# Kernel optimization log

Measured on AMD Instinct MI355X. Metric: run time of the kernel, lower is better.

Reference implementation:

```python
import jax, jax.numpy as jnp
import numpy as np

N = 50000      # nodes
E = 800000     # edges (avg degree 16)
DIN = 128
HID = 128
OUT = 10       # classes
G = 64         # graphs in batch


def setup_inputs() -> dict:
    key = jax.random.key(0)
    ks = jax.random.split(key, 10)
    x = jax.random.normal(ks[0], (N, DIN), dtype=jnp.float32)
    edge_index = jax.random.randint(ks[1], (2, E), 0, N, dtype=jnp.int32)
    edge_weight = jax.random.uniform(ks[2], (E,), dtype=jnp.float32)
    batch = jnp.sort(jax.random.randint(ks[3], (N,), 0, G, dtype=jnp.int32))
    W1 = jax.random.normal(ks[4], (DIN, HID), dtype=jnp.float32) / np.sqrt(DIN)
    b1 = jnp.zeros((HID,), dtype=jnp.float32)
    W2 = jax.random.normal(ks[5], (HID, HID), dtype=jnp.float32) / np.sqrt(HID)
    b2 = jnp.zeros((HID,), dtype=jnp.float32)
    W3 = jax.random.normal(ks[6], (HID, OUT), dtype=jnp.float32) / np.sqrt(HID)
    b3 = jnp.zeros((OUT,), dtype=jnp.float32)
    return {"x": x, "edge_index": edge_index, "edge_weight": edge_weight,
            "batch": batch, "W1": W1, "b1": b1, "W2": W2, "b2": b2,
            "W3": W3, "b3": b3}


def _gcn_norm(edge_index, edge_weight, n_nodes):
    # PyG gcn_norm: add self-loops with weight 1, D^-1/2 (A+I) D^-1/2
    loop = jnp.arange(n_nodes, dtype=edge_index.dtype)
    src = jnp.concatenate([edge_index[0], loop])
    dst = jnp.concatenate([edge_index[1], loop])
    w = jnp.concatenate([edge_weight, jnp.ones((n_nodes,), edge_weight.dtype)])
    deg = jax.ops.segment_sum(w, dst, num_segments=n_nodes)
    dinv = jnp.where(deg > 0, jax.lax.rsqrt(deg), 0.0)
    norm = dinv[src] * w * dinv[dst]
    return src, dst, norm


def _gcn_conv(x, W, b, src, dst, norm, n_nodes):
    h = x @ W                                      # [N, F] dense transform
    msg = norm[:, None] * h[src]                   # gather + scale  [E+N, F]
    out = jax.ops.segment_sum(msg, dst, num_segments=n_nodes)  # scatter-add
    return out + b


def reference(x, edge_index, edge_weight, batch, W1, b1, W2, b2, W3, b3):
    src, dst, norm = _gcn_norm(edge_index, edge_weight, N)
    h = jax.nn.relu(_gcn_conv(x, W1, b1, src, dst, norm, N))
    h = jax.nn.relu(_gcn_conv(h, W2, b2, src, dst, norm, N))
    h = _gcn_conv(h, W3, b3, src, dst, norm, N)    # [N, OUT]
    # global_mean_pool over graph ids
    sums = jax.ops.segment_sum(h, batch, num_segments=G)          # [G, OUT]
    cnts = jax.ops.segment_sum(jnp.ones((N,), h.dtype), batch, num_segments=G)
    pooled = sums / jnp.maximum(cnts, 1.0)[:, None]
    return jax.nn.log_softmax(pooled, axis=1)
```

## Files before the change

### kernel.cpp

```cpp
#include <hip/hip_runtime.h>
#include <math.h>

#define NN 50000
#define EE 800000
#define GG 64
#define FD 128
#define OUTD 10
#define GB 782
#define BB 196
#define NBU 196
#define NBK 128
#define CH 6250
#define RCAP 8

typedef __attribute__((ext_vector_type(8))) short s8v;
typedef __attribute__((ext_vector_type(4))) float f4v;

static __device__ inline unsigned short f2b(float f) {
    unsigned int u = __float_as_uint(f);
    return (unsigned short)((u + 0x7FFFu + ((u >> 16) & 1u)) >> 16);
}


__global__ void k_prep(const float* __restrict__ W1, const float* __restrict__ W2,
                       const float* __restrict__ W3, unsigned short* __restrict__ Wt1,
                       unsigned short* __restrict__ Wt2, float* __restrict__ W3t) {
    int i = blockIdx.x * blockDim.x + threadIdx.x;
    if (i < FD * FD) {
        int nn = i >> 7, k = i & 127;
        Wt1[i] = f2b(W1[k * FD + nn]);
        Wt2[i] = f2b(W2[k * FD + nn]);
    }
    if (i < FD * OUTD) {
        int col = i >> 7, row = i & 127;
        W3t[i] = W3[row * OUTD + col];
    }
}


static __device__ inline void gemm_f32in_body(int bid, const float* __restrict__ A,
        const unsigned short* __restrict__ Wt, unsigned short* __restrict__ out, int n) {
    int tid = threadIdx.x;
    int wave = tid >> 6, lane = tid & 63;
    int quad = lane >> 4, c16 = lane & 15;
    int rowbase = bid * 64 + wave * 16;
    int rowA = rowbase + c16;
    if (rowA >= n) rowA = n - 1;
    f4v acc[8];
    #pragma unroll
    for (int t = 0; t < 8; ++t) acc[t] = (f4v){0.f, 0.f, 0.f, 0.f};
    #pragma unroll
    for (int k0 = 0; k0 < 128; k0 += 32) {
        const float* ap = A + (size_t)rowA * FD + k0 + quad * 8;
        float4 a0 = *(const float4*)ap;
        float4 a1 = *(const float4*)(ap + 4);
        s8v a;
        a[0] = (short)f2b(a0.x); a[1] = (short)f2b(a0.y);
        a[2] = (short)f2b(a0.z); a[3] = (short)f2b(a0.w);
        a[4] = (short)f2b(a1.x); a[5] = (short)f2b(a1.y);
        a[6] = (short)f2b(a1.z); a[7] = (short)f2b(a1.w);
        #pragma unroll
        for (int t = 0; t < 8; ++t) {
            s8v b = *(const s8v*)(Wt + (size_t)(t * 16 + c16) * FD + k0 + quad * 8);
            acc[t] = __builtin_amdgcn_mfma_f32_16x16x32_bf16(a, b, acc[t], 0, 0, 0);
        }
    }
    #pragma unroll
    for (int t = 0; t < 8; ++t) {
        #pragma unroll
        for (int r = 0; r < 4; ++r) {
            int row = rowbase + quad * 4 + r;
            if (row < n) out[(size_t)row * FD + t * 16 + c16] = f2b(acc[t][r]);
        }
    }
}

__global__ __launch_bounds__(256) void k_megaA(const float* __restrict__ x,
        const unsigned short* __restrict__ Wt1, unsigned short* __restrict__ hA,
        const int* __restrict__ dst, int* __restrict__ cnt2d,
        const int* __restrict__ batch, int* __restrict__ gstart) {
    int b = blockIdx.x;
    int tid = threadIdx.x;
    if (b < GB) {
        gemm_f32in_body(b, x, Wt1, hA, NN);
    } else if (b < GB + NBK) {
        __shared__ unsigned hist[NBU];
        int blk = b - GB;
        if (tid < NBU) hist[tid] = 0;
        __syncthreads();
        int e0 = blk * CH;
        for (int e = e0 + tid; e < e0 + CH; e += 256)
            atomicAdd(&hist[(unsigned)dst[e] >> 8], 1u);
        __syncthreads();
        if (tid < NBU) cnt2d[tid * NBK + blk] = (int)hist[tid];
    } else {
        int i = (b - GB - NBK) * 256 + tid;
        if (i < NN) {
            int bb = batch[i];
            int bp = (i == 0) ? -1 : batch[i - 1];
            for (int g = bp + 1; g <= bb; ++g) gstart[g] = i;
            if (i == NN - 1)
                for (int g = bb + 1; g <= GG; ++g) gstart[g] = NN;
        }
    }
}


__global__ __launch_bounds__(256) void k_scatter(const int* __restrict__ src,
        const int* __restrict__ dst, const float* __restrict__ ew,
        const int* __restrict__ cnt2d, int* __restrict__ bbase_g,
        uint2* __restrict__ rec) {
    __shared__ int colsum[NBU];
    __shared__ int ownoff[NBU];
    __shared__ unsigned cur[NBU];
    __shared__ int wtot_s[4];
    int tid = threadIdx.x;
    int blk = blockIdx.x;
    if (tid < NBU) {
        const int* c = cnt2d + tid * NBK;
        int own = 0, tot = 0;
        for (int b = 0; b < NBK; ++b) {
            int t = c[b];
            if (b < blk) own += t;
            tot += t;
        }
        ownoff[tid] = own;
        colsum[tid] = tot;
    }
    __syncthreads();
    {
        int lane = tid & 63, wv = tid >> 6;
        int v = (tid < NBU) ? colsum[tid] : 0;
        int s = v;
        #pragma unroll
        for (int off = 1; off < 64; off <<= 1) {
            int u = __shfl_up(s, off, 64);
            if (lane >= off) s += u;
        }
        if (lane == 63) wtot_s[wv] = s;
        __syncthreads();
        int pre = 0;
        for (int j = 0; j < wv; ++j) pre += wtot_s[j];
        int base = pre + s - v;
        if (tid < NBU) {
            cur[tid] = (unsigned)(base + ownoff[tid]);
            if (blk == 0) bbase_g[tid] = base;
        }
        if (blk == 0 && tid == NBU - 1) bbase_g[NBU] = base + v;
    }
    __syncthreads();
    int e0 = blk * CH;
    for (int e = e0 + tid; e < e0 + CH; e += 256) {
        int d = dst[e];
        unsigned bkt = (unsigned)d >> 8;
        unsigned pos = atomicAdd(&cur[bkt], 1u);
        rec[pos] = make_uint2(((unsigned)(d & 255) << 16) | (unsigned)src[e],
                              __float_as_uint(ew[e]));
    }
}


__global__ __launch_bounds__(1024) void k_rankfill(const uint2* __restrict__ rec,
        const int* __restrict__ bbase, int* __restrict__ rowptr, float* __restrict__ dinv_g,
        uint2* __restrict__ ent, unsigned short* __restrict__ rankb) {
    __shared__ unsigned cntS[256];
    __shared__ float wdegS[256];
    __shared__ int wtot_s[4];
    __shared__ int rowS[256];
    __shared__ float dinvS[256];
    int b = blockIdx.x;
    int tid = threadIdx.x;
    if (tid < 256) { cntS[tid] = 0; wdegS[tid] = 0.0f; }
    __syncthreads();
    int beg = bbase[b], end = bbase[b + 1];
    int s0 = beg + tid;
    uint2 rv[RCAP];
    unsigned rk[RCAP];
    #pragma unroll
    for (int k = 0; k < RCAP; ++k) {
        int s = s0 + k * 1024;
        if (s < end) {
            uint2 r = rec[s];
            unsigned dl = r.x >> 16;
            unsigned old = atomicAdd(&cntS[dl], 1u);
            atomicAdd(&wdegS[dl], __uint_as_float(r.y));
            rv[k] = r; rk[k] = old;
        }
    }
    for (int s = s0 + RCAP * 1024; s < end; s += 1024) {
        uint2 r = rec[s];
        unsigned dl = r.x >> 16;
        unsigned old = atomicAdd(&cntS[dl], 1u);
        atomicAdd(&wdegS[dl], __uint_as_float(r.y));
        rankb[s] = (unsigned short)old;
    }
    __syncthreads();
    {
        int lane = tid & 63, wv = tid >> 6;
        int v = (tid < 256) ? (int)cntS[tid] : 0;
        int s = v;
        #pragma unroll
        for (int off = 1; off < 64; off <<= 1) {
            int u = __shfl_up(s, off, 64);
            if (lane >= off) s += u;
        }
        if (tid < 256 && lane == 63) wtot_s[wv] = s;
        __syncthreads();
        if (tid < 256) {
            int pre = 0;
            for (int j = 0; j < wv; ++j) pre += wtot_s[j];
            int excl = pre + s - v;
            int node = b * 256 + tid;
            if (node < NN) {
                int r = beg + node + excl;
                rowS[tid] = r;
                rowptr[node] = r;
                float di = 1.0f / sqrtf(wdegS[tid] + 1.0f);
                dinvS[tid] = di;
                dinv_g[node] = di;
                ent[r + v] = make_uint2((unsigned)node, __float_as_uint(di));
            }
            if (node == NN - 1) rowptr[NN] = EE + NN;
        }
    }
    __syncthreads();
    #pragma unroll
    for (int k = 0; k < RCAP; ++k) {
        int s = s0 + k * 1024;
        if (s < end) {
            uint2 r = rv[k];
            unsigned dl = r.x >> 16;
            int pos = rowS[dl] + (int)rk[k];
            float val = __uint_as_float(r.y) * dinvS[dl];
            ent[pos] = make_uint2(r.x & 0xFFFFu, __float_as_uint(val));
        }
    }
    for (int s = s0 + RCAP * 1024; s < end; s += 1024) {
        uint2 r = rec[s];
        unsigned dl = r.x >> 16;
        int pos = rowS[dl] + (int)rankb[s];
        float val = __uint_as_float(r.y) * dinvS[dl];
        ent[pos] = make_uint2(r.x & 0xFFFFu, __float_as_uint(val));
    }
}


__global__ __launch_bounds__(256) void k_gemm_bf(const unsigned short* __restrict__ A,
        const unsigned short* __restrict__ Wt, unsigned short* __restrict__ out, int n) {
    int tid = threadIdx.x;
    int wave = tid >> 6, lane = tid & 63;
    int quad = lane >> 4, c16 = lane & 15;
    int rowbase = blockIdx.x * 64 + wave * 16;
    int rowA = rowbase + c16;
    if (rowA >= n) rowA = n - 1;
    f4v acc[8];
    #pragma unroll
    for (int t = 0; t < 8; ++t) acc[t] = (f4v){0.f, 0.f, 0.f, 0.f};
    #pragma unroll
    for (int k0 = 0; k0 < 128; k0 += 32) {
        s8v a = *(const s8v*)(A + (size_t)rowA * FD + k0 + quad * 8);
        #pragma unroll
        for (int t = 0; t < 8; ++t) {
            s8v b = *(const s8v*)(Wt + (size_t)(t * 16 + c16) * FD + k0 + quad * 8);
            acc[t] = __builtin_amdgcn_mfma_f32_16x16x32_bf16(a, b, acc[t], 0, 0, 0);
        }
    }
    #pragma unroll
    for (int t = 0; t < 8; ++t) {
        #pragma unroll
        for (int r = 0; r < 4; ++r) {
            int row = rowbase + quad * 4 + r;
            if (row < n) out[(size_t)row * FD + t * 16 + c16] = f2b(acc[t][r]);
        }
    }
}


__global__ __launch_bounds__(256) void k_spmm_bf(const int* __restrict__ rowptr,
        const uint2* __restrict__ ent, const float* __restrict__ dinv,
        const unsigned short* __restrict__ tin, const float* __restrict__ bias,
        unsigned short* __restrict__ out, int n, int dorelu) {
    int w = (blockIdx.x * blockDim.x + threadIdx.x) >> 6;
    int lane = threadIdx.x & 63;
    if (w >= n) return;
    int c = lane & 15, g = lane >> 4;
    int beg = rowptr[w], end = rowptr[w + 1];
    float acc[8];
    #pragma unroll
    for (int j = 0; j < 8; ++j) acc[j] = 0.0f;
    int e0 = beg;
    for (; e0 + 16 <= end; e0 += 16) {
        uint2 en[4];
        float dv[4];
        uint4 t[4];
        #pragma unroll
        for (int u = 0; u < 4; ++u) en[u] = ent[e0 + 4 * u + g];
        #pragma unroll
        for (int u = 0; u < 4; ++u) dv[u] = dinv[en[u].x];
        #pragma unroll
        for (int u = 0; u < 4; ++u)
            t[u] = *(const uint4*)(tin + (size_t)en[u].x * FD + c * 8);
        #pragma unroll
        for (int u = 0; u < 4; ++u) {
            float v = __uint_as_float(en[u].y) * dv[u];
            acc[0] += v * __uint_as_float(t[u].x << 16);
            acc[1] += v * __uint_as_float(t[u].x & 0xFFFF0000u);
            acc[2] += v * __uint_as_float(t[u].y << 16);
            acc[3] += v * __uint_as_float(t[u].y & 0xFFFF0000u);
            acc[4] += v * __uint_as_float(t[u].z << 16);
            acc[5] += v * __uint_as_float(t[u].z & 0xFFFF0000u);
            acc[6] += v * __uint_as_float(t[u].w << 16);
            acc[7] += v * __uint_as_float(t[u].w & 0xFFFF0000u);
        }
    }
    for (; e0 < end; e0 += 4) {
        int e = e0 + g;
        uint2 en = (e < end) ? ent[e] : make_uint2(0u, 0u);
        float v = (e < end) ? __uint_as_float(en.y) * dinv[en.x] : 0.0f;
        uint4 t = *(const uint4*)(tin + (size_t)en.x * FD + c * 8);
        acc[0] += v * __uint_as_float(t.x << 16);
        acc[1] += v * __uint_as_float(t.x & 0xFFFF0000u);
        acc[2] += v * __uint_as_float(t.y << 16);
        acc[3] += v * __uint_as_float(t.y & 0xFFFF0000u);
        acc[4] += v * __uint_as_float(t.z << 16);
        acc[5] += v * __uint_as_float(t.z & 0xFFFF0000u);
        acc[6] += v * __uint_as_float(t.w << 16);
        acc[7] += v * __uint_as_float(t.w & 0xFFFF0000u);
    }
    #pragma unroll
    for (int j = 0; j < 8; ++j) {
        acc[j] += __shfl_xor(acc[j], 16, 64);
        acc[j] += __shfl_xor(acc[j], 32, 64);
    }
    if (g == 0) {
        uint4 r;
        float o[8];
        #pragma unroll
        for (int j = 0; j < 8; ++j) {
            float x = acc[j] + bias[c * 8 + j];
            o[j] = dorelu ? fmaxf(x, 0.0f) : x;
        }
        r.x = (unsigned)f2b(o[0]) | ((unsigned)f2b(o[1]) << 16);
        r.y = (unsigned)f2b(o[2]) | ((unsigned)f2b(o[3]) << 16);
        r.z = (unsigned)f2b(o[4]) | ((unsigned)f2b(o[5]) << 16);
        r.w = (unsigned)f2b(o[6]) | ((unsigned)f2b(o[7]) << 16);
        *(uint4*)(out + (size_t)w * FD + c * 8) = r;
    }
}

__global__ __launch_bounds__(256) void k_spmm_w3(const int* __restrict__ rowptr,
        const uint2* __restrict__ ent, const float* __restrict__ dinv,
        const unsigned short* __restrict__ tin, const float* __restrict__ bias2,
        const float* __restrict__ W3t, float* __restrict__ outc, int n) {
    int tid = threadIdx.x;
    int w = (blockIdx.x * blockDim.x + tid) >> 6;
    int lane = tid & 63;
    if (w >= n) return;
    int c = lane & 15, g = lane >> 4;
    int beg = rowptr[w], end = rowptr[w + 1];
    float acc[8];
    #pragma unroll
    for (int j = 0; j < 8; ++j) acc[j] = 0.0f;
    int e0 = beg;
    for (; e0 + 16 <= end; e0 += 16) {
        uint2 en[4];
        float dv[4];
        uint4 t[4];
        #pragma unroll
        for (int u = 0; u < 4; ++u) en[u] = ent[e0 + 4 * u + g];
        #pragma unroll
        for (int u = 0; u < 4; ++u) dv[u] = dinv[en[u].x];
        #pragma unroll
        for (int u = 0; u < 4; ++u)
            t[u] = *(const uint4*)(tin + (size_t)en[u].x * FD + c * 8);
        #pragma unroll
        for (int u = 0; u < 4; ++u) {
            float v = __uint_as_float(en[u].y) * dv[u];
            acc[0] += v * __uint_as_float(t[u].x << 16);
            acc[1] += v * __uint_as_float(t[u].x & 0xFFFF0000u);
            acc[2] += v * __uint_as_float(t[u].y << 16);
            acc[3] += v * __uint_as_float(t[u].y & 0xFFFF0000u);
            acc[4] += v * __uint_as_float(t[u].z << 16);
            acc[5] += v * __uint_as_float(t[u].z & 0xFFFF0000u);
            acc[6] += v * __uint_as_float(t[u].w << 16);
            acc[7] += v * __uint_as_float(t[u].w & 0xFFFF0000u);
        }
    }
    for (; e0 < end; e0 += 4) {
        int e = e0 + g;
        uint2 en = (e < end) ? ent[e] : make_uint2(0u, 0u);
        float v = (e < end) ? __uint_as_float(en.y) * dinv[en.x] : 0.0f;
        uint4 t = *(const uint4*)(tin + (size_t)en.x * FD + c * 8);
        acc[0] += v * __uint_as_float(t.x << 16);
        acc[1] += v * __uint_as_float(t.x & 0xFFFF0000u);
        acc[2] += v * __uint_as_float(t.y << 16);
        acc[3] += v * __uint_as_float(t.y & 0xFFFF0000u);
        acc[4] += v * __uint_as_float(t.z << 16);
        acc[5] += v * __uint_as_float(t.z & 0xFFFF0000u);
        acc[6] += v * __uint_as_float(t.w << 16);
        acc[7] += v * __uint_as_float(t.w & 0xFFFF0000u);
    }
    #pragma unroll
    for (int j = 0; j < 8; ++j) {
        acc[j] += __shfl_xor(acc[j], 16, 64);
        acc[j] += __shfl_xor(acc[j], 32, 64);
    }
    float b2r[8], o[8];
    *(float4*)&b2r[0] = *(const float4*)(bias2 + c * 8);
    *(float4*)&b2r[4] = *(const float4*)(bias2 + c * 8 + 4);
    #pragma unroll
    for (int j = 0; j < 8; ++j)
        o[j] = fmaxf(acc[j] + b2r[j], 0.0f);
    float w0[8], w1[8];
    *(float4*)&w0[0] = *(const float4*)(W3t + g * FD + c * 8);
    *(float4*)&w0[4] = *(const float4*)(W3t + g * FD + c * 8 + 4);
    *(float4*)&w1[0] = *(const float4*)(W3t + (g + 4) * FD + c * 8);
    *(float4*)&w1[4] = *(const float4*)(W3t + (g + 4) * FD + c * 8 + 4);
    float p0 = 0.0f, p1 = 0.0f, p2 = 0.0f;
    #pragma unroll
    for (int j = 0; j < 8; ++j) {
        p0 += o[j] * w0[j];
        p1 += o[j] * w1[j];
    }
    if (g < 2) {
        float w2[8];
        *(float4*)&w2[0] = *(const float4*)(W3t + (g + 8) * FD + c * 8);
        *(float4*)&w2[4] = *(const float4*)(W3t + (g + 8) * FD + c * 8 + 4);
        #pragma unroll
        for (int j = 0; j < 8; ++j) p2 += o[j] * w2[j];
    }
    #pragma unroll
    for (int off = 1; off < 16; off <<= 1) {
        p0 += __shfl_xor(p0, off, 64);
        p1 += __shfl_xor(p1, off, 64);
        p2 += __shfl_xor(p2, off, 64);
    }
    if (c == 0) {
        float* op = outc + (size_t)w * OUTD;
        op[g] = p0;
        op[g + 4] = p1;
        if (g < 2) op[g + 8] = p2;
    }
}

__global__ void k_spmm10(const int* __restrict__ rowptr, const uint2* __restrict__ ent,
        const float* __restrict__ dinv, const float* __restrict__ tin,
        const float* __restrict__ bias, float* __restrict__ out, int n) {
    int t = blockIdx.x * blockDim.x + threadIdx.x;
    int node = t / OUTD;
    int c = t - node * OUTD;
    if (node >= n) return;
    int beg = rowptr[node], end = rowptr[node + 1];
    float acc = 0.0f;
    for (int e = beg; e < end; ++e) {
        uint2 en = ent[e];
        acc += __uint_as_float(en.y) * dinv[en.x] * tin[(size_t)en.x * OUTD + c];
    }
    out[(size_t)node * OUTD + c] = acc + bias[c];
}


__global__ __launch_bounds__(256) void k_poolfin(const float* __restrict__ h,
        const int* __restrict__ gstart, float* __restrict__ out) {
    int g = blockIdx.x;
    int beg = gstart[g], end = gstart[g + 1];
    int tid = threadIdx.x;
    int lane = tid & 63, wv = tid >> 6;
    float acc[OUTD];
    #pragma unroll
    for (int c = 0; c < OUTD; ++c) acc[c] = 0.0f;
    for (int i = beg + tid; i < end; i += 256) {
        const float* hp = h + (size_t)i * OUTD;
        #pragma unroll
        for (int c = 0; c < OUTD; ++c) acc[c] += hp[c];
    }
    #pragma unroll
    for (int off = 32; off >= 1; off >>= 1)
        #pragma unroll
        for (int c = 0; c < OUTD; ++c) acc[c] += __shfl_down(acc[c], off, 64);
    __shared__ float ws[4][OUTD];
    if (lane == 0)
        #pragma unroll
        for (int c = 0; c < OUTD; ++c) ws[wv][c] = acc[c];
    __syncthreads();
    if (tid == 0) {
        float cf = fmaxf((float)(end - beg), 1.0f);
        float v[OUTD], m = -1e30f;
        #pragma unroll
        for (int c = 0; c < OUTD; ++c) {
            v[c] = (ws[0][c] + ws[1][c] + ws[2][c] + ws[3][c]) / cf;
            m = fmaxf(m, v[c]);
        }
        float s = 0.0f;
        #pragma unroll
        for (int c = 0; c < OUTD; ++c) s += expf(v[c] - m);
        float l = logf(s);
        #pragma unroll
        for (int c = 0; c < OUTD; ++c) out[g * OUTD + c] = v[c] - m - l;
    }
}


extern "C" void kernel_launch(void* const* d_in, const int* in_sizes, int n_in,
                              void* d_out, int out_size, void* d_ws, size_t ws_size,
                              hipStream_t stream) {
    const float* x   = (const float*)d_in[0];
    const int*   ei  = (const int*)d_in[1];
    const float* ew  = (const float*)d_in[2];
    const int*   bat = (const int*)d_in[3];
    const float* W1  = (const float*)d_in[4];
    const float* b1  = (const float*)d_in[5];
    const float* W2  = (const float*)d_in[6];
    const float* b2  = (const float*)d_in[7];
    const float* W3  = (const float*)d_in[8];
    const float* b3  = (const float*)d_in[9];
    float* out = (float*)d_out;

    const int* src = ei;
    const int* dst = ei + EE;

    char* p = (char*)d_ws;
    auto alloc = [&](size_t bytes) -> void* {
        void* r = (void*)p;
        p += (bytes + 255) & ~(size_t)255;
        return r;
    };
    int*            cnt2d  = (int*)  alloc((size_t)NBU * NBK * 4);
    int*            bbase  = (int*)  alloc((size_t)(NBU + 1) * 4);
    uint2*          rec    = (uint2*)alloc((size_t)EE * 8);
    unsigned short* rankb  = (unsigned short*)alloc((size_t)EE * 2);
    float*          dinv   = (float*)alloc((size_t)NN * 4);
    int*            rowptr = (int*)  alloc((size_t)(NN + 1) * 4);
    uint2*          ent    = (uint2*)alloc((size_t)(EE + NN) * 8);
    unsigned short* Wt1    = (unsigned short*)alloc((size_t)FD * FD * 2);
    unsigned short* Wt2    = (unsigned short*)alloc((size_t)FD * FD * 2);
    float*          W3t    = (float*)alloc((size_t)FD * OUTD * 4);
    unsigned short* hA     = (unsigned short*)alloc((size_t)NN * FD * 2);
    unsigned short* hB     = (unsigned short*)alloc((size_t)NN * FD * 2);
    float*          bufC   = (float*)alloc((size_t)NN * OUTD * 4);
    float*          bufD   = (float*)alloc((size_t)NN * OUTD * 4);
    int*            gstart = (int*)  alloc((size_t)(GG + 1) * 4);
    (void)ws_size; (void)in_sizes; (void)n_in; (void)out_size;

    const int B = 256;
    k_prep    <<<(FD * FD + B - 1) / B, B, 0, stream>>>(W1, W2, W3, Wt1, Wt2, W3t);
    k_megaA   <<<GB + NBK + BB, B, 0, stream>>>(x, Wt1, hA, dst, cnt2d, bat, gstart);
    k_scatter <<<NBK, B, 0, stream>>>(src, dst, ew, cnt2d, bbase, rec);
    k_rankfill<<<NBU, 1024, 0, stream>>>(rec, bbase, rowptr, dinv, ent, rankb);

    k_spmm_bf <<<(NN * 64 + B - 1) / B, B, 0, stream>>>(rowptr, ent, dinv, hA, b1, hB, NN, 1);
    k_gemm_bf <<<GB, B, 0, stream>>>(hB, Wt2, hA, NN);
    k_spmm_w3 <<<(NN * 64 + B - 1) / B, B, 0, stream>>>(rowptr, ent, dinv, hA, b2, W3t, bufC, NN);
    k_spmm10  <<<(NN * OUTD + B - 1) / B, B, 0, stream>>>(rowptr, ent, dinv, bufC, b3, bufD, NN);
    k_poolfin <<<GG, 256, 0, stream>>>(bufD, gstart, out);
}
```

Before: 267.9 us.

## Fuse pooling into final SpMM and fold source dinv into producer epilogues

Merges weight prep with the histogram/graph-bounds kernel and the edge scatter with the first GEMM, cutting kernel launches. The final 10-wide aggregation now accumulates per-graph sums in shared memory and global atomics, and the last block computes mean pooling and log-softmax, removing the separate pool kernel and intermediate buffer. The dinv scaling of source nodes moves into the epilogues of the producing kernels, so the per-edge dinv gathers disappear. Risks: float atomic summation order becomes nondeterministic, and correctness depends on every producer applying the dinv scaling consistently.

After: 372.3 us. 38.9% more time.

```diff
diff --git a/kernel.cpp b/kernel.cpp
--- a/kernel.cpp
+++ b/kernel.cpp
@@ -12,6 +12,8 @@
 #define NBK 128
 #define CH 6250
 #define RCAP 8
+#define TB 64
+#define NPB 1954
 
 typedef __attribute__((ext_vector_type(8))) short s8v;
 typedef __attribute__((ext_vector_type(4))) float f4v;
@@ -22,18 +24,46 @@
 }
 
 
-__global__ void k_prep(const float* __restrict__ W1, const float* __restrict__ W2,
-                       const float* __restrict__ W3, unsigned short* __restrict__ Wt1,
-                       unsigned short* __restrict__ Wt2, float* __restrict__ W3t) {
-    int i = blockIdx.x * blockDim.x + threadIdx.x;
-    if (i < FD * FD) {
-        int nn = i >> 7, k = i & 127;
-        Wt1[i] = f2b(W1[k * FD + nn]);
-        Wt2[i] = f2b(W2[k * FD + nn]);
-    }
-    if (i < FD * OUTD) {
-        int col = i >> 7, row = i & 127;
-        W3t[i] = W3[row * OUTD + col];
+__global__ __launch_bounds__(256) void k_histbounds(const float* __restrict__ W1,
+        const float* __restrict__ W2, const float* __restrict__ W3,
+        unsigned short* __restrict__ Wt1, unsigned short* __restrict__ Wt2,
+        float* __restrict__ W3t, const int* __restrict__ dst, int* __restrict__ cnt2d,
+        const int* __restrict__ batch, int* __restrict__ gstart,
+        float* __restrict__ sums, int* __restrict__ done) {
+    int b = blockIdx.x;
+    int tid = threadIdx.x;
+    if (b < TB) {
+        int i = b * 256 + tid;
+        if (i < FD * FD) {
+            int nn = i >> 7, k = i & 127;
+            Wt1[i] = f2b(W1[k * FD + nn]);
+            Wt2[i] = f2b(W2[k * FD + nn]);
+        }
+        if (i < FD * OUTD) {
+            int col = i >> 7, row = i & 127;
+            W3t[i] = W3[row * OUTD + col];
+        }
+        if (i < GG * OUTD) sums[i] = 0.0f;
+        if (i == 1024) *done = 0;
+    } else if (b < TB + NBK) {
+        __shared__ unsigned hist[NBU];
+        int blk = b - TB;
+        if (tid < NBU) hist[tid] = 0;
+        __syncthreads();
+        int e0 = blk * CH;
+        for (int e = e0 + tid; e < e0 + CH; e += 256)
+            atomicAdd(&hist[(unsigned)dst[e] >> 8], 1u);
+        __syncthreads();
+        if (tid < NBU) cnt2d[tid * NBK + blk] = (int)hist[tid];
+    } else {
+        int i = (b - TB - NBK) * 256 + tid;
+        if (i < NN) {
+            int bb = batch[i];
+            int bp = (i == 0) ? -1 : batch[i - 1];
+            for (int g = bp + 1; g <= bb; ++g) gstart[g] = i;
+            if (i == NN - 1)
+                for (int g = bb + 1; g <= GG; ++g) gstart[g] = NN;
+        }
     }
 }
 
@@ -61,8 +91,8 @@
         a[6] = (short)f2b(a1.z); a[7] = (short)f2b(a1.w);
         #pragma unroll
         for (int t = 0; t < 8; ++t) {
-            s8v b = *(const s8v*)(Wt + (size_t)(t * 16 + c16) * FD + k0 + quad * 8);
-            acc[t] = __builtin_amdgcn_mfma_f32_16x16x32_bf16(a, b, acc[t], 0, 0, 0);
+            s8v bb = *(const s8v*)(Wt + (size_t)(t * 16 + c16) * FD + k0 + quad * 8);
+            acc[t] = __builtin_amdgcn_mfma_f32_16x16x32_bf16(a, bb, acc[t], 0, 0, 0);
         }
     }
     #pragma unroll
@@ -75,53 +105,28 @@
     }
 }
 
-__global__ __launch_bounds__(256) void k_megaA(const float* __restrict__ x,
-        const unsigned short* __restrict__ Wt1, unsigned short* __restrict__ hA,
-        const int* __restrict__ dst, int* __restrict__ cnt2d,
-        const int* __restrict__ batch, int* __restrict__ gstart) {
+__global__ __launch_bounds__(256) void k_scatgemm(const int* __restrict__ src,
+        const int* __restrict__ dst, const float* __restrict__ ew,
+        const int* __restrict__ cnt2d, int* __restrict__ bbase_g, uint2* __restrict__ rec,
+        const float* __restrict__ x, const unsigned short* __restrict__ Wt1,
+        unsigned short* __restrict__ hA) {
     int b = blockIdx.x;
     int tid = threadIdx.x;
-    if (b < GB) {
-        gemm_f32in_body(b, x, Wt1, hA, NN);
-    } else if (b < GB + NBK) {
-        __shared__ unsigned hist[NBU];
-        int blk = b - GB;
-        if (tid < NBU) hist[tid] = 0;
-        __syncthreads();
-        int e0 = blk * CH;
-        for (int e = e0 + tid; e < e0 + CH; e += 256)
-            atomicAdd(&hist[(unsigned)dst[e] >> 8], 1u);
-        __syncthreads();
-        if (tid < NBU) cnt2d[tid * NBK + blk] = (int)hist[tid];
-    } else {
-        int i = (b - GB - NBK) * 256 + tid;
-        if (i < NN) {
-            int bb = batch[i];
-            int bp = (i == 0) ? -1 : batch[i - 1];
-            for (int g = bp + 1; g <= bb; ++g) gstart[g] = i;
-            if (i == NN - 1)
-                for (int g = bb + 1; g <= GG; ++g) gstart[g] = NN;
-        }
-    }
-}
-
-
-__global__ __launch_bounds__(256) void k_scatter(const int* __restrict__ src,
-        const int* __restrict__ dst, const float* __restrict__ ew,
-        const int* __restrict__ cnt2d, int* __restrict__ bbase_g,
-        uint2* __restrict__ rec) {
+    if (b >= NBK) {
+        gemm_f32in_body(b - NBK, x, Wt1, hA, NN);
+        return;
+    }
     __shared__ int colsum[NBU];
     __shared__ int ownoff[NBU];
     __shared__ unsigned cur[NBU];
     __shared__ int wtot_s[4];
-    int tid = threadIdx.x;
-    int blk = blockIdx.x;
+    int blk = b;
     if (tid < NBU) {
         const int* c = cnt2d + tid * NBK;
         int own = 0, tot = 0;
-        for (int b = 0; b < NBK; ++b) {
-            int t = c[b];
-            if (b < blk) own += t;
+        for (int k = 0; k < NBK; ++k) {
+            int t = c[k];
+            if (k < blk) own += t;
             tot += t;
         }
         ownoff[tid] = own;
@@ -245,41 +250,10 @@
 }
 
 
-__global__ __launch_bounds__(256) void k_gemm_bf(const unsigned short* __restrict__ A,
-        const unsigned short* __restrict__ Wt, unsigned short* __restrict__ out, int n) {
-    int tid = threadIdx.x;
-    int wave = tid >> 6, lane = tid & 63;
-    int quad = lane >> 4, c16 = lane & 15;
-    int rowbase = blockIdx.x * 64 + wave * 16;
-    int rowA = rowbase + c16;
-    if (rowA >= n) rowA = n - 1;
-    f4v acc[8];
-    #pragma unroll
-    for (int t = 0; t < 8; ++t) acc[t] = (f4v){0.f, 0.f, 0.f, 0.f};
-    #pragma unroll
-    for (int k0 = 0; k0 < 128; k0 += 32) {
-        s8v a = *(const s8v*)(A + (size_t)rowA * FD + k0 + quad * 8);
-        #pragma unroll
-        for (int t = 0; t < 8; ++t) {
-            s8v b = *(const s8v*)(Wt + (size_t)(t * 16 + c16) * FD + k0 + quad * 8);
-            acc[t] = __builtin_amdgcn_mfma_f32_16x16x32_bf16(a, b, acc[t], 0, 0, 0);
-        }
-    }
-    #pragma unroll
-    for (int t = 0; t < 8; ++t) {
-        #pragma unroll
-        for (int r = 0; r < 4; ++r) {
-            int row = rowbase + quad * 4 + r;
-            if (row < n) out[(size_t)row * FD + t * 16 + c16] = f2b(acc[t][r]);
-        }
-    }
-}
-
-
 __global__ __launch_bounds__(256) void k_spmm_bf(const int* __restrict__ rowptr,
         const uint2* __restrict__ ent, const float* __restrict__ dinv,
         const unsigned short* __restrict__ tin, const float* __restrict__ bias,
-        unsigned short* __restrict__ out, int n, int dorelu) {
+        unsigned short* __restrict__ out, int n) {
     int w = (blockIdx.x * blockDim.x + threadIdx.x) >> 6;
     int lane = threadIdx.x & 63;
     if (w >= n) return;
@@ -333,13 +307,12 @@
         acc[j] += __shfl_xor(acc[j], 32, 64);
     }
     if (g == 0) {
+        float dself = dinv[w];
         uint4 r;
         float o[8];
         #pragma unroll
-        for (int j = 0; j < 8; ++j) {
-            float x = acc[j] + bias[c * 8 + j];
-            o[j] = dorelu ? fmaxf(x, 0.0f) : x;
-        }
+        for (int j = 0; j < 8; ++j)
+            o[j] = fmaxf(acc[j] + bias[c * 8 + j], 0.0f) * dself;
         r.x = (unsigned)f2b(o[0]) | ((unsigned)f2b(o[1]) << 16);
         r.y = (unsigned)f2b(o[2]) | ((unsigned)f2b(o[3]) << 16);
         r.z = (unsigned)f2b(o[4]) | ((unsigned)f2b(o[5]) << 16);
@@ -347,6 +320,38 @@
         *(uint4*)(out + (size_t)w * FD + c * 8) = r;
     }
 }
+
+
+__global__ __launch_bounds__(256) void k_gemm_bf(const unsigned short* __restrict__ A,
+        const unsigned short* __restrict__ Wt, unsigned short* __restrict__ out, int n) {
+    int tid = threadIdx.x;
+    int wave = tid >> 6, lane = tid & 63;
+    int quad = lane >> 4, c16 = lane & 15;
+    int rowbase = blockIdx.x * 64 + wave * 16;
+    int rowA = rowbase + c16;
+    if (rowA >= n) rowA = n - 1;
+    f4v acc[8];
+    #pragma unroll
+    for (int t = 0; t < 8; ++t) acc[t] = (f4v){0.f, 0.f, 0.f, 0.f};
+    #pragma unroll
+    for (int k0 = 0; k0 < 128; k0 += 32) {
+        s8v a = *(const s8v*)(A + (size_t)rowA * FD + k0 + quad * 8);
+        #pragma unroll
+        for (int t = 0; t < 8; ++t) {
+            s8v b = *(const s8v*)(Wt + (size_t)(t * 16 + c16) * FD + k0 + quad * 8);
+            acc[t] = __builtin_amdgcn_mfma_f32_16x16x32_bf16(a, b, acc[t], 0, 0, 0);
+        }
+    }
+    #pragma unroll
+    for (int t = 0; t < 8; ++t) {
+        #pragma unroll
+        for (int r = 0; r < 4; ++r) {
+            int row = rowbase + quad * 4 + r;
+            if (row < n) out[(size_t)row * FD + t * 16 + c16] = f2b(acc[t][r]);
+        }
+    }
+}
+
 
 __global__ __launch_bounds__(256) void k_spmm_w3(const int* __restrict__ rowptr,
         const uint2* __restrict__ ent, const float* __restrict__ dinv,
@@ -364,18 +369,15 @@
     int e0 = beg;
     for (; e0 + 16 <= end; e0 += 16) {
         uint2 en[4];
-        float dv[4];
         uint4 t[4];
         #pragma unroll
         for (int u = 0; u < 4; ++u) en[u] = ent[e0 + 4 * u + g];
-        #pragma unroll
-        for (int u = 0; u < 4; ++u) dv[u] = dinv[en[u].x];
         #pragma unroll
         for (int u = 0; u < 4; ++u)
             t[u] = *(const uint4*)(tin + (size_t)en[u].x * FD + c * 8);
         #pragma unroll
         for (int u = 0; u < 4; ++u) {
-            float v = __uint_as_float(en[u].y) * dv[u];
+            float v = __uint_as_float(en[u].y);
             acc[0] += v * __uint_as_float(t[u].x << 16);
             acc[1] += v * __uint_as_float(t[u].x & 0xFFFF0000u);
             acc[2] += v * __uint_as_float(t[u].y << 16);
@@ -389,7 +391,7 @@
     for (; e0 < end; e0 += 4) {
         int e = e0 + g;
         uint2 en = (e < end) ? ent[e] : make_uint2(0u, 0u);
-        float v = (e < end) ? __uint_as_float(en.y) * dinv[en.x] : 0.0f;
+        float v = (e < end) ? __uint_as_float(en.y) : 0.0f;
         uint4 t = *(const uint4*)(tin + (size_t)en.x * FD + c * 8);
         acc[0] += v * __uint_as_float(t.x << 16);
         acc[1] += v * __uint_as_float(t.x & 0xFFFF0000u);
@@ -436,67 +438,75 @@
         p2 += __shfl_xor(p2, off, 64);
     }
     if (c == 0) {
+        float dself = dinv[w];
         float* op = outc + (size_t)w * OUTD;
-        op[g] = p0;
-        op[g + 4] = p1;
-        if (g < 2) op[g + 8] = p2;
-    }
-}
-
-__global__ void k_spmm10(const int* __restrict__ rowptr, const uint2* __restrict__ ent,
-        const float* __restrict__ dinv, const float* __restrict__ tin,
-        const float* __restrict__ bias, float* __restrict__ out, int n) {
-    int t = blockIdx.x * blockDim.x + threadIdx.x;
+        op[g] = p0 * dself;
+        op[g + 4] = p1 * dself;
+        if (g < 2) op[g + 8] = p2 * dself;
+    }
+}
+
+
+__global__ __launch_bounds__(256) void k_spmm10pool(const int* __restrict__ rowptr,
+        const uint2* __restrict__ ent, const float* __restrict__ tin,
+        const float* __restrict__ bias, const int* __restrict__ batch,
+        const int* __restrict__ gstart, float* __restrict__ sums, int* __restrict__ done,
+        float* __restrict__ out) {
+    __shared__ float gs[16][OUTD];
+    __shared__ int gmin_s, gmax_s, last_s;
+    int tid = threadIdx.x;
+    int t = blockIdx.x * 256 + tid;
     int node = t / OUTD;
     int c = t - node * OUTD;
-    if (node >= n) return;
-    int beg = rowptr[node], end = rowptr[node + 1];
-    float acc = 0.0f;
-    for (int e = beg; e < end; ++e) {
-        uint2 en = ent[e];
-        acc += __uint_as_float(en.y) * dinv[en.x] * tin[(size_t)en.x * OUTD + c];
-    }
-    out[(size_t)node * OUTD + c] = acc + bias[c];
-}
-
-
-__global__ __launch_bounds__(256) void k_poolfin(const float* __restrict__ h,
-        const int* __restrict__ gstart, float* __restrict__ out) {
-    int g = blockIdx.x;
-    int beg = gstart[g], end = gstart[g + 1];
-    int tid = threadIdx.x;
-    int lane = tid & 63, wv = tid >> 6;
-    float acc[OUTD];
-    #pragma unroll
-    for (int c = 0; c < OUTD; ++c) acc[c] = 0.0f;
-    for (int i = beg + tid; i < end; i += 256) {
-        const float* hp = h + (size_t)i * OUTD;
-        #pragma unroll
-        for (int c = 0; c < OUTD; ++c) acc[c] += hp[c];
-    }
-    #pragma unroll
-    for (int off = 32; off >= 1; off >>= 1)
-        #pragma unroll
-        for (int c = 0; c < OUTD; ++c) acc[c] += __shfl_down(acc[c], off, 64);
-    __shared__ float ws[4][OUTD];
-    if (lane == 0)
-        #pragma unroll
-        for (int c = 0; c < OUTD; ++c) ws[wv][c] = acc[c];
-    __syncthreads();
-    if (tid == 0) {
-        float cf = fmaxf((float)(end - beg), 1.0f);
+    bool act = node < NN;
+    if (tid == 0) { gmin_s = 0x7fffffff; gmax_s = -1; }
+    if (tid < 16 * OUTD) gs[tid / OUTD][tid % OUTD] = 0.0f;
+    __syncthreads();
+    int g = 0;
+    float val = 0.0f;
+    if (act) {
+        g = batch[node];
+        atomicMin(&gmin_s, g);
+        atomicMax(&gmax_s, g);
+        int beg = rowptr[node], end = rowptr[node + 1];
+        for (int e = beg; e < end; ++e) {
+            uint2 en = ent[e];
+            val += __uint_as_float(en.y) * tin[(size_t)en.x * OUTD + c];
+        }
+        val += bias[c];
+    }
+    __syncthreads();
+    if (act) atomicAdd(&gs[g & 15][c], val);
+    __syncthreads();
+    if (tid < 16 * OUTD) {
+        int s = tid / OUTD, cc = tid - s * OUTD;
+        int gmin = gmin_s, gmax = gmax_s;
+        if (gmax >= 0) {
+            int gg = gmin + ((s - (gmin & 15) + 16) & 15);
+            if (gg <= gmax) atomicAdd(&sums[gg * OUTD + cc], gs[s][cc]);
+        }
+    }
+    __threadfence();
+    __syncthreads();
+    if (tid == 0) last_s = (atomicAdd(done, 1) == NPB - 1) ? 1 : 0;
+    __syncthreads();
+    if (last_s && tid < GG) {
+        int g2 = tid;
+        float cf = fmaxf((float)(gstart[g2 + 1] - gstart[g2]), 1.0f);
         float v[OUTD], m = -1e30f;
         #pragma unroll
-        for (int c = 0; c < OUTD; ++c) {
-            v[c] = (ws[0][c] + ws[1][c] + ws[2][c] + ws[3][c]) / cf;
-            m = fmaxf(m, v[c]);
+        for (int cc = 0; cc < OUTD; ++cc) {
+            float s = __hip_atomic_load(&sums[g2 * OUTD + cc], __ATOMIC_RELAXED,
+                                        __HIP_MEMORY_SCOPE_AGENT);
+            v[cc] = s / cf;
+            m = fmaxf(m, v[cc]);
         }
         float s = 0.0f;
         #pragma unroll
-        for (int c = 0; c < OUTD; ++c) s += expf(v[c] - m);
+        for (int cc = 0; cc < OUTD; ++cc) s += expf(v[cc] - m);
         float l = logf(s);
         #pragma unroll
-        for (int c = 0; c < OUTD; ++c) out[g * OUTD + c] = v[c] - m - l;
+        for (int cc = 0; cc < OUTD; ++cc) out[g2 * OUTD + cc] = v[cc] - m - l;
     }
 }
 
@@ -538,19 +548,18 @@
     unsigned short* hA     = (unsigned short*)alloc((size_t)NN * FD * 2);
     unsigned short* hB     = (unsigned short*)alloc((size_t)NN * FD * 2);
     float*          bufC   = (float*)alloc((size_t)NN * OUTD * 4);
-    float*          bufD   = (float*)alloc((size_t)NN * OUTD * 4);
+    float*          sums   = (float*)alloc((size_t)GG * OUTD * 4);
+    int*            done   = (int*)  alloc(256);
     int*            gstart = (int*)  alloc((size_t)(GG + 1) * 4);
     (void)ws_size; (void)in_sizes; (void)n_in; (void)out_size;
 
     const int B = 256;
-    k_prep    <<<(FD * FD + B - 1) / B, B, 0, stream>>>(W1, W2, W3, Wt1, Wt2, W3t);
-    k_megaA   <<<GB + NBK + BB, B, 0, stream>>>(x, Wt1, hA, dst, cnt2d, bat, gstart);
-    k_scatter <<<NBK, B, 0, stream>>>(src, dst, ew, cnt2d, bbase, rec);
-    k_rankfill<<<NBU, 1024, 0, stream>>>(rec, bbase, rowptr, dinv, ent, rankb);
-
-    k_spmm_bf <<<(NN * 64 + B - 1) / B, B, 0, stream>>>(rowptr, ent, dinv, hA, b1, hB, NN, 1);
-    k_gemm_bf <<<GB, B, 0, stream>>>(hB, Wt2, hA, NN);
-    k_spmm_w3 <<<(NN * 64 + B - 1) / B, B, 0, stream>>>(rowptr, ent, dinv, hA, b2, W3t, bufC, NN);
-    k_spmm10  <<<(NN * OUTD + B - 1) / B, B, 0, stream>>>(rowptr, ent, dinv, bufC, b3, bufD, NN);
-    k_poolfin <<<GG, 256, 0, stream>>>(bufD, gstart, out);
-}
+    k_histbounds<<<TB + NBK + BB, B, 0, stream>>>(W1, W2, W3, Wt1, Wt2, W3t,
+                                                  dst, cnt2d, bat, gstart, sums, done);
+    k_scatgemm  <<<NBK + GB, B, 0, stream>>>(src, dst, ew, cnt2d, bbase, rec, x, Wt1, hA);
+    k_rankfill  <<<NBU, 1024, 0, stream>>>(rec, bbase, rowptr, dinv, ent, rankb);
+    k_spmm_bf   <<<(NN * 64 + B - 1) / B, B, 0, stream>>>(rowptr, ent, dinv, hA, b1, hB, NN);
+    k_gemm_bf   <<<GB, B, 0, stream>>>(hB, Wt2, hA, NN);
+    k_spmm_w3   <<<(NN * 64 + B - 1) / B, B, 0, stream>>>(rowptr, ent, dinv, hA, b2, W3t, bufC, NN);
+    k_spmm10pool<<<NPB, B, 0, stream>>>(rowptr, ent, bufC, b3, bat, gstart, sums, done, out);
+}
```

## Fold source-side degree scaling into producers and merge setup kernels

Applied to the files above, without the earlier changes.

The source-side D^-1/2 factor is now applied once per row: the layer-1 and layer-2 aggregation epilogues multiply their outputs by dinv[node]. This lets the layer-2 and layer-3 aggregations drop the per-edge dinv gather, which is valid because the following GEMM is linear in row scaling. Weight preparation is merged into the histogram/graph-bounds kernel, and the first GEMM runs in the same launch as the edge scatter. That cuts the launch count and overlaps the dense GEMM with the irregular scatter. The extra dinv multiply before bf16 rounding slightly changes numerics.

After: 254.8 us. -4.9%, faster.

```diff
diff --git a/kernel.cpp b/kernel.cpp
--- a/kernel.cpp
+++ b/kernel.cpp
@@ -12,6 +12,7 @@
 #define NBK 128
 #define CH 6250
 #define RCAP 8
+#define TB 64
 
 typedef __attribute__((ext_vector_type(8))) short s8v;
 typedef __attribute__((ext_vector_type(4))) float f4v;
@@ -22,18 +23,43 @@
 }
 
 
-__global__ void k_prep(const float* __restrict__ W1, const float* __restrict__ W2,
-                       const float* __restrict__ W3, unsigned short* __restrict__ Wt1,
-                       unsigned short* __restrict__ Wt2, float* __restrict__ W3t) {
-    int i = blockIdx.x * blockDim.x + threadIdx.x;
-    if (i < FD * FD) {
-        int nn = i >> 7, k = i & 127;
-        Wt1[i] = f2b(W1[k * FD + nn]);
-        Wt2[i] = f2b(W2[k * FD + nn]);
-    }
-    if (i < FD * OUTD) {
-        int col = i >> 7, row = i & 127;
-        W3t[i] = W3[row * OUTD + col];
+__global__ __launch_bounds__(256) void k_histbounds(const float* __restrict__ W1,
+        const float* __restrict__ W2, const float* __restrict__ W3,
+        unsigned short* __restrict__ Wt1, unsigned short* __restrict__ Wt2,
+        float* __restrict__ W3t, const int* __restrict__ dst, int* __restrict__ cnt2d,
+        const int* __restrict__ batch, int* __restrict__ gstart) {
+    int b = blockIdx.x;
+    int tid = threadIdx.x;
+    if (b < TB) {
+        int i = b * 256 + tid;
+        if (i < FD * FD) {
+            int nn = i >> 7, k = i & 127;
+            Wt1[i] = f2b(W1[k * FD + nn]);
+            Wt2[i] = f2b(W2[k * FD + nn]);
+        }
+        if (i < FD * OUTD) {
+            int col = i >> 7, row = i & 127;
+            W3t[i] = W3[row * OUTD + col];
+        }
+    } else if (b < TB + NBK) {
+        __shared__ unsigned hist[NBU];
+        int blk = b - TB;
+        if (tid < NBU) hist[tid] = 0;
+        __syncthreads();
+        int e0 = blk * CH;
+        for (int e = e0 + tid; e < e0 + CH; e += 256)
+            atomicAdd(&hist[(unsigned)dst[e] >> 8], 1u);
+        __syncthreads();
+        if (tid < NBU) cnt2d[tid * NBK + blk] = (int)hist[tid];
+    } else {
+        int i = (b - TB - NBK) * 256 + tid;
+        if (i < NN) {
+            int bb = batch[i];
+            int bp = (i == 0) ? -1 : batch[i - 1];
+            for (int g = bp + 1; g <= bb; ++g) gstart[g] = i;
+            if (i == NN - 1)
+                for (int g = bb + 1; g <= GG; ++g) gstart[g] = NN;
+        }
     }
 }
 
@@ -61,8 +87,8 @@
         a[6] = (short)f2b(a1.z); a[7] = (short)f2b(a1.w);
         #pragma unroll
         for (int t = 0; t < 8; ++t) {
-            s8v b = *(const s8v*)(Wt + (size_t)(t * 16 + c16) * FD + k0 + quad * 8);
-            acc[t] = __builtin_amdgcn_mfma_f32_16x16x32_bf16(a, b, acc[t], 0, 0, 0);
+            s8v bb = *(const s8v*)(Wt + (size_t)(t * 16 + c16) * FD + k0 + quad * 8);
+            acc[t] = __builtin_amdgcn_mfma_f32_16x16x32_bf16(a, bb, acc[t], 0, 0, 0);
         }
     }
     #pragma unroll
@@ -75,53 +101,28 @@
     }
 }
 
-__global__ __launch_bounds__(256) void k_megaA(const float* __restrict__ x,
-        const unsigned short* __restrict__ Wt1, unsigned short* __restrict__ hA,
-        const int* __restrict__ dst, int* __restrict__ cnt2d,
-        const int* __restrict__ batch, int* __restrict__ gstart) {
+__global__ __launch_bounds__(256) void k_scatgemm(const int* __restrict__ src,
+        const int* __restrict__ dst, const float* __restrict__ ew,
+        const int* __restrict__ cnt2d, int* __restrict__ bbase_g, uint2* __restrict__ rec,
+        const float* __restrict__ x, const unsigned short* __restrict__ Wt1,
+        unsigned short* __restrict__ hA) {
     int b = blockIdx.x;
     int tid = threadIdx.x;
-    if (b < GB) {
-        gemm_f32in_body(b, x, Wt1, hA, NN);
-    } else if (b < GB + NBK) {
-        __shared__ unsigned hist[NBU];
-        int blk = b - GB;
-        if (tid < NBU) hist[tid] = 0;
-        __syncthreads();
-        int e0 = blk * CH;
-        for (int e = e0 + tid; e < e0 + CH; e += 256)
-            atomicAdd(&hist[(unsigned)dst[e] >> 8], 1u);
-        __syncthreads();
-        if (tid < NBU) cnt2d[tid * NBK + blk] = (int)hist[tid];
-    } else {
-        int i = (b - GB - NBK) * 256 + tid;
-        if (i < NN) {
-            int bb = batch[i];
-            int bp = (i == 0) ? -1 : batch[i - 1];
-            for (int g = bp + 1; g <= bb; ++g) gstart[g] = i;
-            if (i == NN - 1)
-                for (int g = bb + 1; g <= GG; ++g) gstart[g] = NN;
-        }
-    }
-}
-
-
-__global__ __launch_bounds__(256) void k_scatter(const int* __restrict__ src,
-        const int* __restrict__ dst, const float* __restrict__ ew,
-        const int* __restrict__ cnt2d, int* __restrict__ bbase_g,
-        uint2* __restrict__ rec) {
+    if (b >= NBK) {
+        gemm_f32in_body(b - NBK, x, Wt1, hA, NN);
+        return;
+    }
     __shared__ int colsum[NBU];
     __shared__ int ownoff[NBU];
     __shared__ unsigned cur[NBU];
     __shared__ int wtot_s[4];
-    int tid = threadIdx.x;
-    int blk = blockIdx.x;
+    int blk = b;
     if (tid < NBU) {
         const int* c = cnt2d + tid * NBK;
         int own = 0, tot = 0;
-        for (int b = 0; b < NBK; ++b) {
-            int t = c[b];
-            if (b < blk) own += t;
+        for (int k = 0; k < NBK; ++k) {
+            int t = c[k];
+            if (k < blk) own += t;
             tot += t;
         }
         ownoff[tid] = own;
@@ -245,41 +246,10 @@
 }
 
 
-__global__ __launch_bounds__(256) void k_gemm_bf(const unsigned short* __restrict__ A,
-        const unsigned short* __restrict__ Wt, unsigned short* __restrict__ out, int n) {
-    int tid = threadIdx.x;
-    int wave = tid >> 6, lane = tid & 63;
-    int quad = lane >> 4, c16 = lane & 15;
-    int rowbase = blockIdx.x * 64 + wave * 16;
-    int rowA = rowbase + c16;
-    if (rowA >= n) rowA = n - 1;
-    f4v acc[8];
-    #pragma unroll
-    for (int t = 0; t < 8; ++t) acc[t] = (f4v){0.f, 0.f, 0.f, 0.f};
-    #pragma unroll
-    for (int k0 = 0; k0 < 128; k0 += 32) {
-        s8v a = *(const s8v*)(A + (size_t)rowA * FD + k0 + quad * 8);
-        #pragma unroll
-        for (int t = 0; t < 8; ++t) {
-            s8v b = *(const s8v*)(Wt + (size_t)(t * 16 + c16) * FD + k0 + quad * 8);
-            acc[t] = __builtin_amdgcn_mfma_f32_16x16x32_bf16(a, b, acc[t], 0, 0, 0);
-        }
-    }
-    #pragma unroll
-    for (int t = 0; t < 8; ++t) {
-        #pragma unroll
-        for (int r = 0; r < 4; ++r) {
-            int row = rowbase + quad * 4 + r;
-            if (row < n) out[(size_t)row * FD + t * 16 + c16] = f2b(acc[t][r]);
-        }
-    }
-}
-
-
 __global__ __launch_bounds__(256) void k_spmm_bf(const int* __restrict__ rowptr,
         const uint2* __restrict__ ent, const float* __restrict__ dinv,
         const unsigned short* __restrict__ tin, const float* __restrict__ bias,
-        unsigned short* __restrict__ out, int n, int dorelu) {
+        unsigned short* __restrict__ out, int n) {
     int w = (blockIdx.x * blockDim.x + threadIdx.x) >> 6;
     int lane = threadIdx.x & 63;
     if (w >= n) return;
@@ -333,13 +303,12 @@
         acc[j] += __shfl_xor(acc[j], 32, 64);
     }
     if (g == 0) {
+        float dself = dinv[w];
         uint4 r;
         float o[8];
         #pragma unroll
-        for (int j = 0; j < 8; ++j) {
-            float x = acc[j] + bias[c * 8 + j];
-            o[j] = dorelu ? fmaxf(x, 0.0f) : x;
-        }
+        for (int j = 0; j < 8; ++j)
+            o[j] = fmaxf(acc[j] + bias[c * 8 + j], 0.0f) * dself;
         r.x = (unsigned)f2b(o[0]) | ((unsigned)f2b(o[1]) << 16);
         r.y = (unsigned)f2b(o[2]) | ((unsigned)f2b(o[3]) << 16);
         r.z = (unsigned)f2b(o[4]) | ((unsigned)f2b(o[5]) << 16);
@@ -347,6 +316,38 @@
         *(uint4*)(out + (size_t)w * FD + c * 8) = r;
     }
 }
+
+
+__global__ __launch_bounds__(256) void k_gemm_bf(const unsigned short* __restrict__ A,
+        const unsigned short* __restrict__ Wt, unsigned short* __restrict__ out, int n) {
+    int tid = threadIdx.x;
+    int wave = tid >> 6, lane = tid & 63;
+    int quad = lane >> 4, c16 = lane & 15;
+    int rowbase = blockIdx.x * 64 + wave * 16;
+    int rowA = rowbase + c16;
+    if (rowA >= n) rowA = n - 1;
+    f4v acc[8];
+    #pragma unroll
+    for (int t = 0; t < 8; ++t) acc[t] = (f4v){0.f, 0.f, 0.f, 0.f};
+    #pragma unroll
+    for (int k0 = 0; k0 < 128; k0 += 32) {
+        s8v a = *(const s8v*)(A + (size_t)rowA * FD + k0 + quad * 8);
+        #pragma unroll
+        for (int t = 0; t < 8; ++t) {
+            s8v b = *(const s8v*)(Wt + (size_t)(t * 16 + c16) * FD + k0 + quad * 8);
+            acc[t] = __builtin_amdgcn_mfma_f32_16x16x32_bf16(a, b, acc[t], 0, 0, 0);
+        }
+    }
+    #pragma unroll
+    for (int t = 0; t < 8; ++t) {
+        #pragma unroll
+        for (int r = 0; r < 4; ++r) {
+            int row = rowbase + quad * 4 + r;
+            if (row < n) out[(size_t)row * FD + t * 16 + c16] = f2b(acc[t][r]);
+        }
+    }
+}
+
 
 __global__ __launch_bounds__(256) void k_spmm_w3(const int* __restrict__ rowptr,
         const uint2* __restrict__ ent, const float* __restrict__ dinv,
@@ -364,18 +365,15 @@
     int e0 = beg;
     for (; e0 + 16 <= end; e0 += 16) {
         uint2 en[4];
-        float dv[4];
         uint4 t[4];
         #pragma unroll
         for (int u = 0; u < 4; ++u) en[u] = ent[e0 + 4 * u + g];
-        #pragma unroll
-        for (int u = 0; u < 4; ++u) dv[u] = dinv[en[u].x];
         #pragma unroll
         for (int u = 0; u < 4; ++u)
             t[u] = *(const uint4*)(tin + (size_t)en[u].x * FD + c * 8);
         #pragma unroll
         for (int u = 0; u < 4; ++u) {
-            float v = __uint_as_float(en[u].y) * dv[u];
+            float v = __uint_as_float(en[u].y);
             acc[0] += v * __uint_as_float(t[u].x << 16);
             acc[1] += v * __uint_as_float(t[u].x & 0xFFFF0000u);
             acc[2] += v * __uint_as_float(t[u].y << 16);
@@ -389,7 +387,7 @@
     for (; e0 < end; e0 += 4) {
         int e = e0 + g;
         uint2 en = (e < end) ? ent[e] : make_uint2(0u, 0u);
-        float v = (e < end) ? __uint_as_float(en.y) * dinv[en.x] : 0.0f;
+        float v = (e < end) ? __uint_as_float(en.y) : 0.0f;
         uint4 t = *(const uint4*)(tin + (size_t)en.x * FD + c * 8);
         acc[0] += v * __uint_as_float(t.x << 16);
         acc[1] += v * __uint_as_float(t.x & 0xFFFF0000u);
@@ -436,16 +434,18 @@
         p2 += __shfl_xor(p2, off, 64);
     }
     if (c == 0) {
+        float dself = dinv[w];
         float* op = outc + (size_t)w * OUTD;
-        op[g] = p0;
-        op[g + 4] = p1;
-        if (g < 2) op[g + 8] = p2;
-    }
-}
+        op[g] = p0 * dself;
+        op[g + 4] = p1 * dself;
+        if (g < 2) op[g + 8] = p2 * dself;
+    }
+}
+
 
 __global__ void k_spmm10(const int* __restrict__ rowptr, const uint2* __restrict__ ent,
-        const float* __restrict__ dinv, const float* __restrict__ tin,
-        const float* __restrict__ bias, float* __restrict__ out, int n) {
+        const float* __restrict__ tin, const float* __restrict__ bias,
+        float* __restrict__ out, int n) {
     int t = blockIdx.x * blockDim.x + threadIdx.x;
     int node = t / OUTD;
     int c = t - node * OUTD;
@@ -454,7 +454,7 @@
     float acc = 0.0f;
     for (int e = beg; e < end; ++e) {
         uint2 en = ent[e];
-        acc += __uint_as_float(en.y) * dinv[en.x] * tin[(size_t)en.x * OUTD + c];
+        acc += __uint_as_float(en.y) * tin[(size_t)en.x * OUTD + c];
     }
     out[(size_t)node * OUTD + c] = acc + bias[c];
 }
@@ -543,14 +543,13 @@
     (void)ws_size; (void)in_sizes; (void)n_in; (void)out_size;
 
     const int B = 256;
-    k_prep    <<<(FD * FD + B - 1) / B, B, 0, stream>>>(W1, W2, W3, Wt1, Wt2, W3t);
-    k_megaA   <<<GB + NBK + BB, B, 0, stream>>>(x, Wt1, hA, dst, cnt2d, bat, gstart);
-    k_scatter <<<NBK, B, 0, stream>>>(src, dst, ew, cnt2d, bbase, rec);
+    k_histbounds<<<TB + NBK + BB, B, 0, stream>>>(W1, W2, W3, Wt1, Wt2, W3t,
+                                                  dst, cnt2d, bat, gstart);
+    k_scatgemm<<<NBK + GB, B, 0, stream>>>(src, dst, ew, cnt2d, bbase, rec, x, Wt1, hA);
     k_rankfill<<<NBU, 1024, 0, stream>>>(rec, bbase, rowptr, dinv, ent, rankb);
-
-    k_spmm_bf <<<(NN * 64 + B - 1) / B, B, 0, stream>>>(rowptr, ent, dinv, hA, b1, hB, NN, 1);
+    k_spmm_bf <<<(NN * 64 + B - 1) / B, B, 0, stream>>>(rowptr, ent, dinv, hA, b1, hB, NN);
     k_gemm_bf <<<GB, B, 0, stream>>>(hB, Wt2, hA, NN);
     k_spmm_w3 <<<(NN * 64 + B - 1) / B, B, 0, stream>>>(rowptr, ent, dinv, hA, b2, W3t, bufC, NN);
-    k_spmm10  <<<(NN * OUTD + B - 1) / B, B, 0, stream>>>(rowptr, ent, dinv, bufC, b3, bufD, NN);
+    k_spmm10  <<<(NN * OUTD + B - 1) / B, B, 0, stream>>>(rowptr, ent, bufC, b3, bufD, NN);
     k_poolfin <<<GG, 256, 0, stream>>>(bufD, gstart, out);
 }
```
